# Performance work log

Measured on AMD Instinct MI355X. Metric: run time of the kernel, lower is better.

## Reference

```python
import jax, jax.numpy as jnp
import numpy as np

N = 50000
E = 1600000

def _glorot(k, shp):
    lim = np.sqrt(6.0 / (shp[0] + shp[1])).astype(np.float32)
    return jax.random.uniform(k, shp, jnp.float32, -lim, lim)

def setup_inputs() -> dict:
    key = jax.random.key(0)
    ks = jax.random.split(key, 8)
    return {
        "x": jax.random.normal(ks[0], (N, 640), jnp.float32),
        "edges": jax.random.randint(ks[1], (E, 2), 0, N),  # [E,2] (src, dst)
        "Wb": _glorot(ks[2], (640, 64)),  "bb": jnp.zeros((64,), jnp.float32),
        "Ws1": _glorot(ks[3], (64, 64)),  "bs1": jnp.zeros((64,), jnp.float32),
        "Ws2": _glorot(ks[4], (64, 640)), "bs2": jnp.zeros((640,), jnp.float32),
        "Ww1": _glorot(ks[5], (64, 64)),  "bw1": jnp.zeros((64,), jnp.float32),
        "Ww2": _glorot(ks[6], (64, 640)), "bw2": jnp.zeros((640,), jnp.float32),
    }

def _gcn_conv(x, W, b, src, dst, dinv):
    # PyG GCNConv: x' = D^{-1/2}(A+I)D^{-1/2} x W + b (self-loops included)
    h = x @ W  # [N, out]
    coef = dinv[src] * dinv[dst]  # symmetric norm per edge
    agg = jax.ops.segment_sum(h[src] * coef[:, None], dst, num_segments=x.shape[0])
    agg = agg + h * (dinv * dinv)[:, None]  # self-loop contribution
    return agg + b

def reference(x, edges, Wb, bb, Ws1, bs1, Ws2, bs2, Ww1, bw1, Ww2, bw2):
    src, dst = edges[:, 0], edges[:, 1]
    # degree includes the added self-loop
    deg = jax.ops.segment_sum(jnp.ones_like(dst, jnp.float32), dst, num_segments=x.shape[0]) + 1.0
    dinv = jax.lax.rsqrt(deg)
    xb = jax.nn.relu(_gcn_conv(x, Wb, bb, src, dst, dinv))
    xs = jax.nn.relu(_gcn_conv(xb, Ws1, bs1, src, dst, dinv))
    xs = jax.nn.relu(_gcn_conv(xs, Ws2, bs2, src, dst, dinv))
    xw = jax.nn.relu(_gcn_conv(xb, Ww1, bw1, src, dst, dinv))
    xw = jax.nn.relu(_gcn_conv(xw, Ww2, bw2, src, dst, dinv))
    return (xs, xw)
```

## Files before the change

### kernel.cpp

```cpp
#include <hip/hip_runtime.h>


__global__ void zero_int_kernel(int* __restrict__ p, int n) {
    int i = blockIdx.x * blockDim.x + threadIdx.x;
    if (i < n) p[i] = 0;
}

__global__ void hist_kernel(const int* __restrict__ edges, int* __restrict__ cnt, int E) {
    int e = blockIdx.x * blockDim.x + threadIdx.x;
    if (e < E) atomicAdd(&cnt[edges[2 * e + 1]], 1);
}

__global__ __launch_bounds__(1024)
void scan_block_kernel(const int* __restrict__ cnt, int* __restrict__ excl,
                       int* __restrict__ blocksum, float* __restrict__ dinv, int N) {
    __shared__ int s[1024];
    int tid = threadIdx.x;
    int i = blockIdx.x * 1024 + tid;
    int v = (i < N) ? cnt[i] : 0;
    if (i < N) dinv[i] = rsqrtf((float)v + 1.0f);
    s[tid] = v;
    __syncthreads();
    for (int off = 1; off < 1024; off <<= 1) {
        int t = (tid >= off) ? s[tid - off] : 0;
        __syncthreads();
        s[tid] += t;
        __syncthreads();
    }
    if (i < N) excl[i] = s[tid] - v;
    if (tid == 1023) blocksum[blockIdx.x] = s[1023];
}

__global__ void scan_partials_kernel(int* __restrict__ blocksum, int nb) {
    if (blockIdx.x == 0 && threadIdx.x == 0) {
        int run = 0;
        for (int i = 0; i < nb; ++i) { int v = blocksum[i]; blocksum[i] = run; run += v; }
    }
}

__global__ void scan_finalize_kernel(int* __restrict__ row_start, const int* __restrict__ blocksum,
                                     int* __restrict__ cursor, int N, int E) {
    int i = blockIdx.x * blockDim.x + threadIdx.x;
    if (i < N) {
        int v = row_start[i] + blocksum[i >> 10];
        row_start[i] = v;
        cursor[i] = v;
    }
    if (i == N) row_start[N] = E;
}

__global__ void build_csr_kernel(const int* __restrict__ edges, int* __restrict__ cursor,
                                 int* __restrict__ csr_src, int E) {
    int e = blockIdx.x * blockDim.x + threadIdx.x;
    if (e < E) {
        int s = edges[2 * e], d = edges[2 * e + 1];
        int pos = atomicAdd(&cursor[d], 1);
        csr_src[pos] = s;
    }
}

template <bool BIAS, bool RELU>
__global__ __launch_bounds__(256)
void agg_gather_kernel(const float* __restrict__ in, const float* __restrict__ bias,
                       const int* __restrict__ row_start, const int* __restrict__ csr_src,
                       const float* __restrict__ dinv, float* __restrict__ out, int N) {
    int lane = threadIdx.x & 63;
    int wid  = (blockIdx.x * blockDim.x + threadIdx.x) >> 6;
    int nw   = (gridDim.x * blockDim.x) >> 6;
    float b = BIAS ? bias[lane] : 0.f;
    for (int d = wid; d < N; d += nw) {
        float dv = dinv[d];
        float v = in[(size_t)d * 64 + lane];
        if (BIAS) v += b;
        if (RELU) v = fmaxf(v, 0.f);
        float acc0 = v * dv * dv;
        float acc1 = 0.f;
        int e   = row_start[d];
        int end = row_start[d + 1];
        for (; e + 1 < end; e += 2) {
            int s0 = csr_src[e], s1 = csr_src[e + 1];
            float c0 = dinv[s0] * dv, c1 = dinv[s1] * dv;
            float u0 = in[(size_t)s0 * 64 + lane];
            float u1 = in[(size_t)s1 * 64 + lane];
            if (BIAS) { u0 += b; u1 += b; }
            if (RELU) { u0 = fmaxf(u0, 0.f); u1 = fmaxf(u1, 0.f); }
            acc0 = fmaf(u0, c0, acc0);
            acc1 = fmaf(u1, c1, acc1);
        }
        if (e < end) {
            int s0 = csr_src[e];
            float c0 = dinv[s0] * dv;
            float u0 = in[(size_t)s0 * 64 + lane];
            if (BIAS) u0 += b;
            if (RELU) u0 = fmaxf(u0, 0.f);
            acc0 = fmaf(u0, c0, acc0);
        }
        out[(size_t)d * 64 + lane] = acc0 + acc1;
    }
}

template <bool RELU>
__global__ __launch_bounds__(256)
void gemm_kernel(const float* __restrict__ A, const float* __restrict__ B,
                 const float* __restrict__ bias, float* __restrict__ C,
                 int M, int N, int K) {
    __shared__ float sA[64][33];
    __shared__ float sB[32][64];
    const int tid  = threadIdx.x;
    const int row0 = blockIdx.x * 64;
    const int col0 = blockIdx.y * 64;
    const int tx = tid & 15;
    const int ty = tid >> 4;
    const int tx4 = tx << 2, ty4 = ty << 2;

    float acc[4][4] = {};

    for (int kb = 0; kb < K; kb += 32) {
#pragma unroll
        for (int l = 0; l < 2; ++l) {
            int f  = tid + l * 256;
            int r  = f >> 3;
            int k4 = (f & 7) << 2;
            float4 v = make_float4(0.f, 0.f, 0.f, 0.f);
            int gr = row0 + r;
            if (gr < M) v = *(const float4*)&A[(size_t)gr * K + kb + k4];
            sA[r][k4 + 0] = v.x; sA[r][k4 + 1] = v.y;
            sA[r][k4 + 2] = v.z; sA[r][k4 + 3] = v.w;
        }
#pragma unroll
        for (int l = 0; l < 2; ++l) {
            int f  = tid + l * 256;
            int kr = f >> 4;
            int c4 = (f & 15) << 2;
            *(float4*)&sB[kr][c4] = *(const float4*)&B[(size_t)(kb + kr) * N + col0 + c4];
        }
        __syncthreads();
#pragma unroll
        for (int k = 0; k < 32; ++k) {
            float a0 = sA[ty4 + 0][k];
            float a1 = sA[ty4 + 1][k];
            float a2 = sA[ty4 + 2][k];
            float a3 = sA[ty4 + 3][k];
            float4 b = *(const float4*)&sB[k][tx4];
            acc[0][0] = fmaf(a0, b.x, acc[0][0]); acc[0][1] = fmaf(a0, b.y, acc[0][1]);
            acc[0][2] = fmaf(a0, b.z, acc[0][2]); acc[0][3] = fmaf(a0, b.w, acc[0][3]);
            acc[1][0] = fmaf(a1, b.x, acc[1][0]); acc[1][1] = fmaf(a1, b.y, acc[1][1]);
            acc[1][2] = fmaf(a1, b.z, acc[1][2]); acc[1][3] = fmaf(a1, b.w, acc[1][3]);
            acc[2][0] = fmaf(a2, b.x, acc[2][0]); acc[2][1] = fmaf(a2, b.y, acc[2][1]);
            acc[2][2] = fmaf(a2, b.z, acc[2][2]); acc[2][3] = fmaf(a2, b.w, acc[2][3]);
            acc[3][0] = fmaf(a3, b.x, acc[3][0]); acc[3][1] = fmaf(a3, b.y, acc[3][1]);
            acc[3][2] = fmaf(a3, b.z, acc[3][2]); acc[3][3] = fmaf(a3, b.w, acc[3][3]);
        }
        __syncthreads();
    }

    float4 bv = make_float4(0.f, 0.f, 0.f, 0.f);
    if (bias) bv = *(const float4*)&bias[col0 + tx4];
#pragma unroll
    for (int i = 0; i < 4; ++i) {
        int gr = row0 + ty4 + i;
        if (gr < M) {
            float4 v;
            v.x = acc[i][0] + bv.x; v.y = acc[i][1] + bv.y;
            v.z = acc[i][2] + bv.z; v.w = acc[i][3] + bv.w;
            if (RELU) {
                v.x = fmaxf(v.x, 0.f); v.y = fmaxf(v.y, 0.f);
                v.z = fmaxf(v.z, 0.f); v.w = fmaxf(v.w, 0.f);
            }
            *(float4*)&C[(size_t)gr * N + col0 + tx4] = v;
        }
    }
}

extern "C" void kernel_launch(void* const* d_in, const int* in_sizes, int n_in,
                              void* d_out, int out_size, void* d_ws, size_t ws_size,
                              hipStream_t stream) {
    const float* x     = (const float*)d_in[0];
    const int*   edges = (const int*)d_in[1];
    const float* Wb    = (const float*)d_in[2];
    const float* bb    = (const float*)d_in[3];
    const float* Ws1   = (const float*)d_in[4];
    const float* bs1   = (const float*)d_in[5];
    const float* Ws2   = (const float*)d_in[6];
    const float* bs2   = (const float*)d_in[7];
    const float* Ww1   = (const float*)d_in[8];
    const float* bw1   = (const float*)d_in[9];
    const float* Ww2   = (const float*)d_in[10];
    const float* bw2   = (const float*)d_in[11];

    const int N = in_sizes[0] / 640;
    const int E = in_sizes[1] / 2;

    float* out_xs = (float*)d_out;
    float* out_xw = out_xs + (size_t)N * 640;

    const size_t NP = ((size_t)N + 64) & ~63ULL;
    char* w = (char*)d_ws;
    float* dinv      = (float*)w;              w += NP * 4;
    int*   cnt       = (int*)w;                w += NP * 4;
    int*   row_start = (int*)w;                w += (NP + 64) * 4;
    int*   cursor    = (int*)w;                w += NP * 4;
    int*   csr_src   = (int*)w;                w += ((size_t)E + 64) * 4;
    size_t nf = (size_t)N * 64;
    float* B0 = (float*)w;                     w += nf * 4;
    float* B1 = (float*)w;                     w += nf * 4;
    float* B2 = (float*)w;                     w += nf * 4;

    const dim3 blk(256);
    const int nBlkN   = (N + 255) / 256;
    const int nBlkN1  = (N + 256) / 256;
    const int nBlkE   = (E + 255) / 256;
    const int nScanB  = (N + 1023) / 1024;
    const int rowT    = (N + 63) / 64;
    const int gatherB = (N + 3) / 4;

    zero_int_kernel<<<nBlkN, blk, 0, stream>>>(cnt, N);
    hist_kernel<<<nBlkE, blk, 0, stream>>>(edges, cnt, E);
    scan_block_kernel<<<nScanB, 1024, 0, stream>>>(cnt, row_start, cursor , dinv, N);
    scan_partials_kernel<<<1, 64, 0, stream>>>(cursor, nScanB);
    scan_finalize_kernel<<<nBlkN1, blk, 0, stream>>>(row_start, cursor, cnt , N, E);
    build_csr_kernel<<<nBlkE, blk, 0, stream>>>(edges, cnt, csr_src, E);

    gemm_kernel<false><<<dim3(rowT, 1), blk, 0, stream>>>(x, Wb, nullptr, B0, N, 64, 640);

    agg_gather_kernel<false, false><<<gatherB, blk, 0, stream>>>(B0, nullptr, row_start, csr_src, dinv, B1, N);

    agg_gather_kernel<true, true><<<gatherB, blk, 0, stream>>>(B1, bb, row_start, csr_src, dinv, B2, N);

    gemm_kernel<true><<<dim3(rowT, 1), blk, 0, stream>>>(B2, Ws1, bs1, B0, N, 64, 64);
    agg_gather_kernel<false, false><<<gatherB, blk, 0, stream>>>(B0, nullptr, row_start, csr_src, dinv, B1, N);
    gemm_kernel<true><<<dim3(rowT, 10), blk, 0, stream>>>(B1, Ws2, bs2, out_xs, N, 640, 64);

    gemm_kernel<true><<<dim3(rowT, 1), blk, 0, stream>>>(B2, Ww1, bw1, B0, N, 64, 64);
    agg_gather_kernel<false, false><<<gatherB, blk, 0, stream>>>(B0, nullptr, row_start, csr_src, dinv, B1, N);
    gemm_kernel<true><<<dim3(rowT, 10), blk, 0, stream>>>(B1, Ww2, bw2, out_xw, N, 640, 64);
}
```

Baseline: 1.054 ms.

## Enlarge GEMM register tiles to 128 rows and transpose A in shared memory

Replaces the 64x64 FP32 GEMM tile with a 128-row tile whose column width is templated (64 or 128). Each thread now computes 8x4 or 8x8 outputs, and A is stored transposed in shared memory so it can be read as float4. The K step drops from 32 to 16. The aim is more FMAs per shared-memory load and fewer blocks on the wide 640-column output GEMMs and the K=640 input GEMM, at the cost of more registers and possibly lower occupancy.

```diff
diff --git a/kernel.cpp b/kernel.cpp
--- a/kernel.cpp
+++ b/kernel.cpp
@@ -99,75 +99,95 @@
     }
 }
 
-template <bool RELU>
+template <int TN, bool RELU>
 __global__ __launch_bounds__(256)
-void gemm_kernel(const float* __restrict__ A, const float* __restrict__ B,
-                 const float* __restrict__ bias, float* __restrict__ C,
-                 int M, int N, int K) {
-    __shared__ float sA[64][33];
-    __shared__ float sB[32][64];
+void gemm2_kernel(const float* __restrict__ A, const float* __restrict__ B,
+                  const float* __restrict__ bias, float* __restrict__ C,
+                  int M, int N, int K) {
+    constexpr int NG = TN / 64;
+    __shared__ float sA[16][132];
+    __shared__ float sB[16][TN];
+
     const int tid  = threadIdx.x;
-    const int row0 = blockIdx.x * 64;
-    const int col0 = blockIdx.y * 64;
-    const int tx = tid & 15;
-    const int ty = tid >> 4;
-    const int tx4 = tx << 2, ty4 = ty << 2;
-
-    float acc[4][4] = {};
-
-    for (int kb = 0; kb < K; kb += 32) {
+    const int row0 = blockIdx.x * 128;
+    const int col0 = blockIdx.y * TN;
+    const int tx4  = (tid & 15) << 2;
+    const int ty4  = (tid >> 4) << 2;
+
+    float acc[2][NG][4][4] = {};
+
+    for (int kb = 0; kb < K; kb += 16) {
 #pragma unroll
         for (int l = 0; l < 2; ++l) {
             int f  = tid + l * 256;
-            int r  = f >> 3;
-            int k4 = (f & 7) << 2;
+            int r  = f >> 2;
+            int k4 = (f & 3) << 2;
             float4 v = make_float4(0.f, 0.f, 0.f, 0.f);
             int gr = row0 + r;
             if (gr < M) v = *(const float4*)&A[(size_t)gr * K + kb + k4];
-            sA[r][k4 + 0] = v.x; sA[r][k4 + 1] = v.y;
-            sA[r][k4 + 2] = v.z; sA[r][k4 + 3] = v.w;
-        }
-#pragma unroll
-        for (int l = 0; l < 2; ++l) {
+            sA[k4 + 0][r] = v.x; sA[k4 + 1][r] = v.y;
+            sA[k4 + 2][r] = v.z; sA[k4 + 3][r] = v.w;
+        }
+#pragma unroll
+        for (int l = 0; l < NG; ++l) {
             int f  = tid + l * 256;
-            int kr = f >> 4;
-            int c4 = (f & 15) << 2;
+            int kr = f / (TN / 4);
+            int c4 = (f % (TN / 4)) << 2;
             *(float4*)&sB[kr][c4] = *(const float4*)&B[(size_t)(kb + kr) * N + col0 + c4];
         }
         __syncthreads();
-#pragma unroll
-        for (int k = 0; k < 32; ++k) {
-            float a0 = sA[ty4 + 0][k];
-            float a1 = sA[ty4 + 1][k];
-            float a2 = sA[ty4 + 2][k];
-            float a3 = sA[ty4 + 3][k];
-            float4 b = *(const float4*)&sB[k][tx4];
-            acc[0][0] = fmaf(a0, b.x, acc[0][0]); acc[0][1] = fmaf(a0, b.y, acc[0][1]);
-            acc[0][2] = fmaf(a0, b.z, acc[0][2]); acc[0][3] = fmaf(a0, b.w, acc[0][3]);
-            acc[1][0] = fmaf(a1, b.x, acc[1][0]); acc[1][1] = fmaf(a1, b.y, acc[1][1]);
-            acc[1][2] = fmaf(a1, b.z, acc[1][2]); acc[1][3] = fmaf(a1, b.w, acc[1][3]);
-            acc[2][0] = fmaf(a2, b.x, acc[2][0]); acc[2][1] = fmaf(a2, b.y, acc[2][1]);
-            acc[2][2] = fmaf(a2, b.z, acc[2][2]); acc[2][3] = fmaf(a2, b.w, acc[2][3]);
-            acc[3][0] = fmaf(a3, b.x, acc[3][0]); acc[3][1] = fmaf(a3, b.y, acc[3][1]);
-            acc[3][2] = fmaf(a3, b.z, acc[3][2]); acc[3][3] = fmaf(a3, b.w, acc[3][3]);
-        }
-        __syncthreads();
-    }
-
-    float4 bv = make_float4(0.f, 0.f, 0.f, 0.f);
-    if (bias) bv = *(const float4*)&bias[col0 + tx4];
-#pragma unroll
-    for (int i = 0; i < 4; ++i) {
-        int gr = row0 + ty4 + i;
-        if (gr < M) {
-            float4 v;
-            v.x = acc[i][0] + bv.x; v.y = acc[i][1] + bv.y;
-            v.z = acc[i][2] + bv.z; v.w = acc[i][3] + bv.w;
-            if (RELU) {
-                v.x = fmaxf(v.x, 0.f); v.y = fmaxf(v.y, 0.f);
-                v.z = fmaxf(v.z, 0.f); v.w = fmaxf(v.w, 0.f);
+
+#pragma unroll
+        for (int k = 0; k < 16; ++k) {
+            float4 a0 = *(const float4*)&sA[k][ty4];
+            float4 a1 = *(const float4*)&sA[k][ty4 + 64];
+            float4 b0 = *(const float4*)&sB[k][tx4];
+            float4 b1;
+            if (NG == 2) b1 = *(const float4*)&sB[k][tx4 + 64];
+            const float ar[2][4] = {{a0.x, a0.y, a0.z, a0.w}, {a1.x, a1.y, a1.z, a1.w}};
+#pragma unroll
+            for (int rg = 0; rg < 2; ++rg) {
+#pragma unroll
+                for (int i = 0; i < 4; ++i) {
+                    float a = ar[rg][i];
+                    acc[rg][0][i][0] = fmaf(a, b0.x, acc[rg][0][i][0]);
+                    acc[rg][0][i][1] = fmaf(a, b0.y, acc[rg][0][i][1]);
+                    acc[rg][0][i][2] = fmaf(a, b0.z, acc[rg][0][i][2]);
+                    acc[rg][0][i][3] = fmaf(a, b0.w, acc[rg][0][i][3]);
+                    if (NG == 2) {
+                        acc[rg][1][i][0] = fmaf(a, b1.x, acc[rg][1][i][0]);
+                        acc[rg][1][i][1] = fmaf(a, b1.y, acc[rg][1][i][1]);
+                        acc[rg][1][i][2] = fmaf(a, b1.z, acc[rg][1][i][2]);
+                        acc[rg][1][i][3] = fmaf(a, b1.w, acc[rg][1][i][3]);
+                    }
+                }
             }
-            *(float4*)&C[(size_t)gr * N + col0 + tx4] = v;
+        }
+        __syncthreads();
+    }
+
+#pragma unroll
+    for (int g = 0; g < NG; ++g) {
+        float4 bv = make_float4(0.f, 0.f, 0.f, 0.f);
+        if (bias) bv = *(const float4*)&bias[col0 + g * 64 + tx4];
+#pragma unroll
+        for (int rg = 0; rg < 2; ++rg) {
+#pragma unroll
+            for (int i = 0; i < 4; ++i) {
+                int gr = row0 + rg * 64 + ty4 + i;
+                if (gr < M) {
+                    float4 v;
+                    v.x = acc[rg][g][i][0] + bv.x;
+                    v.y = acc[rg][g][i][1] + bv.y;
+                    v.z = acc[rg][g][i][2] + bv.z;
+                    v.w = acc[rg][g][i][3] + bv.w;
+                    if (RELU) {
+                        v.x = fmaxf(v.x, 0.f); v.y = fmaxf(v.y, 0.f);
+                        v.z = fmaxf(v.z, 0.f); v.w = fmaxf(v.w, 0.f);
+                    }
+                    *(float4*)&C[(size_t)gr * N + col0 + g * 64 + tx4] = v;
+                }
+            }
         }
     }
 }
@@ -211,27 +231,27 @@
     const int nBlkN1  = (N + 256) / 256;
     const int nBlkE   = (E + 255) / 256;
     const int nScanB  = (N + 1023) / 1024;
-    const int rowT    = (N + 63) / 64;
+    const int rowT    = (N + 127) / 128;
     const int gatherB = (N + 3) / 4;
 
     zero_int_kernel<<<nBlkN, blk, 0, stream>>>(cnt, N);
     hist_kernel<<<nBlkE, blk, 0, stream>>>(edges, cnt, E);
-    scan_block_kernel<<<nScanB, 1024, 0, stream>>>(cnt, row_start, cursor , dinv, N);
+    scan_block_kernel<<<nScanB, 1024, 0, stream>>>(cnt, row_start, cursor, dinv, N);
     scan_partials_kernel<<<1, 64, 0, stream>>>(cursor, nScanB);
-    scan_finalize_kernel<<<nBlkN1, blk, 0, stream>>>(row_start, cursor, cnt , N, E);
+    scan_finalize_kernel<<<nBlkN1, blk, 0, stream>>>(row_start, cursor, cnt, N, E);
     build_csr_kernel<<<nBlkE, blk, 0, stream>>>(edges, cnt, csr_src, E);
 
-    gemm_kernel<false><<<dim3(rowT, 1), blk, 0, stream>>>(x, Wb, nullptr, B0, N, 64, 640);
+    gemm2_kernel<64, false><<<dim3(rowT, 1), blk, 0, stream>>>(x, Wb, nullptr, B0, N, 64, 640);
 
     agg_gather_kernel<false, false><<<gatherB, blk, 0, stream>>>(B0, nullptr, row_start, csr_src, dinv, B1, N);
 
     agg_gather_kernel<true, true><<<gatherB, blk, 0, stream>>>(B1, bb, row_start, csr_src, dinv, B2, N);
 
-    gemm_kernel<true><<<dim3(rowT, 1), blk, 0, stream>>>(B2, Ws1, bs1, B0, N, 64, 64);
+    gemm2_kernel<64, true><<<dim3(rowT, 1), blk, 0, stream>>>(B2, Ws1, bs1, B0, N, 64, 64);
     agg_gather_kernel<false, false><<<gatherB, blk, 0, stream>>>(B0, nullptr, row_start, csr_src, dinv, B1, N);
-    gemm_kernel<true><<<dim3(rowT, 10), blk, 0, stream>>>(B1, Ws2, bs2, out_xs, N, 640, 64);
-
-    gemm_kernel<true><<<dim3(rowT, 1), blk, 0, stream>>>(B2, Ww1, bw1, B0, N, 64, 64);
+    gemm2_kernel<128, true><<<dim3(rowT, 5), blk, 0, stream>>>(B1, Ws2, bs2, out_xs, N, 640, 64);
+
+    gemm2_kernel<64, true><<<dim3(rowT, 1), blk, 0, stream>>>(B2, Ww1, bw1, B0, N, 64, 64);
     agg_gather_kernel<false, false><<<gatherB, blk, 0, stream>>>(B0, nullptr, row_start, csr_src, dinv, B1, N);
-    gemm_kernel<true><<<dim3(rowT, 10), blk, 0, stream>>>(B1, Ww2, bw2, out_xw, N, 640, 64);
-}
+    gemm2_kernel<128, true><<<dim3(rowT, 5), blk, 0, stream>>>(B1, Ww2, bw2, out_xw, N, 640, 64);
+}
```

Result: slower. 1.098 ms (+4.2%).
